# Optimization experiments

Hardware: AMD Instinct MI355X
Metric: run time of the kernel (lower is better)

## Reference

```python
import jax, jax.numpy as jnp
import numpy as np

N, B, H, L, FE = 32768, 256, 128, 4, 4
E = 262144


def setup_inputs() -> dict:
    key = jax.random.key(0)
    ks = jax.random.split(key, 16)
    def g(i, shape, scale=0.05):
        return jax.random.normal(ks[i], shape, dtype=jnp.float32) * scale
    return {
        "d": jax.random.uniform(ks[0], (E,), dtype=jnp.float32) * 5.0,
        "src": jax.random.randint(ks[1], (E,), 0, N),
        "dst": jax.random.randint(ks[2], (E,), 0, N),
        "seg": jnp.sort(jax.random.randint(ks[3], (N,), 0, B)),
        "node_emb": g(4, (H,), 1.0),
        "We": g(5, (2 * FE + 1, H)), "be": jnp.zeros((H,), jnp.float32),
        "msg_W1": g(6, (L, 3 * H, H)), "msg_b1": jnp.zeros((L, H), jnp.float32),
        "msg_W2": g(7, (L, H, H)), "msg_b2": jnp.zeros((L, H), jnp.float32),
        "soft_W": g(8, (L, H)), "soft_b": jnp.zeros((L,), jnp.float32),
        "upd_W1": g(9, (L, H, H)), "upd_b1": jnp.zeros((L, H), jnp.float32),
        "upd_W2": g(10, (L, H, H)), "upd_b2": jnp.zeros((L, H), jnp.float32),
        "out_W1": g(11, (H, H)), "out_b1": jnp.zeros((H,), jnp.float32),
        "out_W2": g(12, (H, H)), "out_b2": jnp.zeros((H,), jnp.float32),
    }


def reference(d, src, dst, seg, node_emb, We, be, msg_W1, msg_b1, msg_W2, msg_b2,
              soft_W, soft_b, upd_W1, upd_b1, upd_W2, upd_b2,
              out_W1, out_b1, out_W2, out_b2):
    silu = jax.nn.silu
    # fourier_encode_dist: [E] -> [E, 2*FE+1] = [sin(d/2^k), cos(d/2^k), d]
    scales = 2.0 ** jnp.arange(FE, dtype=d.dtype)
    x = d[:, None] / scales
    de = jnp.concatenate([jnp.sin(x), jnp.cos(x), d[:, None]], axis=-1)
    # edge_input MLP (1 layer, last_activation=SiLU) then extra F.silu in input_edge_func
    e = silu(silu(de @ We + be))                              # [E, H]
    # node_embedding broadcast to all nodes
    feat = jnp.broadcast_to(node_emb, (N, H))
    for l in range(L):
        mi = jnp.concatenate([feat[src], feat[dst], e], axis=-1)        # [E, 3H]
        m = silu(silu(mi @ msg_W1[l] + msg_b1[l]) @ msg_W2[l] + msg_b2[l])  # [E, H]
        e = e + m                                             # edge residual update
        w = jax.nn.sigmoid(m @ soft_W[l] + soft_b[l])[:, None]  # soft edge gate [E,1]
        msum = jax.ops.segment_sum(m * w, dst, num_segments=N)  # reduce to dst nodes
        upd_in = msum + feat
        feat = silu(upd_in @ upd_W1[l] + upd_b1[l]) @ upd_W2[l] + upd_b2[l] + feat
    # node-wise output network (2 layers, last activation None)
    feat = silu(feat @ out_W1 + out_b1) @ out_W2 + out_b2
    # multi-aggregator readout over graphs in batch
    s = jax.ops.segment_sum(feat, seg, num_segments=B)
    cnt = jax.ops.segment_sum(jnp.ones((N, 1), feat.dtype), seg, num_segments=B)
    mean = s / jnp.maximum(cnt, 1.0)
    mx = jax.ops.segment_max(feat, seg, num_segments=B)
    return jnp.concatenate([s, mean, mx], axis=-1)            # [B, 3H]
```

## Files before the change

kernel.cpp:

```cpp
#include <hip/hip_runtime.h>
#include <hip/hip_bf16.h>

#define NN 32768
#define NB 256
#define HD 128
#define NL 4
#define NE 262144

typedef short bf16x8 __attribute__((ext_vector_type(8)));
typedef float f32x4 __attribute__((ext_vector_type(4)));
typedef unsigned short u16;
typedef unsigned int u32;

__device__ __forceinline__ float bf2f(u16 u) {
  return __uint_as_float(((u32)u) << 16);
}
__device__ __forceinline__ u16 f2bf(float f) {
  u32 x = __float_as_uint(f);
  u32 r = x + 0x7FFFu + ((x >> 16) & 1u);
  return (u16)(r >> 16);
}
__device__ __forceinline__ u32 pk2(float a, float b) {
  __hip_bfloat162 h = __float22bfloat162_rn(make_float2(a, b));
  return *reinterpret_cast<u32*>(&h);
}
__device__ __forceinline__ float siluf(float x) {
  return x * __builtin_amdgcn_rcpf(1.0f + __expf(-x));
}
__device__ __forceinline__ float sigf(float x) {
  return __builtin_amdgcn_rcpf(1.0f + __expf(-x));
}
__device__ __forceinline__ u32 ordu(float f) {
  u32 b = __float_as_uint(f);
  return (b & 0x80000000u) ? ~b : (b | 0x80000000u);
}

__device__ __forceinline__ float ldinf(const void* p, size_t i, int mode) {
  return mode ? ((const float*)p)[i] : bf2f(((const u16*)p)[i]);
}
__device__ __forceinline__ u16 ldinb(const void* p, size_t i, int mode) {
  return mode ? f2bf(((const float*)p)[i]) : ((const u16*)p)[i];
}

__global__ void k_detect(const u16* __restrict__ Weraw, int* __restrict__ flag) {
  if (threadIdx.x == 0 && blockIdx.x == 0) {
    int cnt = 0;
    for (int i = 0; i < 256; i++) {
      u16 u = Weraw[2 * i];
      u32 e = (u >> 7) & 0xFFu;
      if (e >= 112u && e <= 126u) cnt++;
    }
    *flag = (cnt >= 128) ? 0 : 1;
  }
}

__global__ void k_v0(const void* __restrict__ nemb, const void* __restrict__ mW1,
                     const int* __restrict__ flagp, float* __restrict__ v0f) {
  const int mode = *flagp;
  const int n = threadIdx.x;
  float s = 0.f;
  for (int k = 0; k < 256; k++)
    s += ldinf(nemb, k & 127, mode) * ldinf(mW1, (size_t)k * HD + n, mode);
  v0f[n] = s;
}

#define PANEL 16384

__global__ __launch_bounds__(256) void k_csr_deg(const int* __restrict__ dstp,
                                                 u32* __restrict__ deg) {
  const int i = blockIdx.x * 256 + threadIdx.x;
  atomicAdd(&deg[dstp[i]], 1u);
}

__global__ __launch_bounds__(1024) void k_csr_scan(const u32* __restrict__ deg,
                                                   int* __restrict__ rowptr,
                                                   int* __restrict__ cursor) {
  __shared__ int part[1024];
  const int t = threadIdx.x;
  int loc[32];
  int s = 0;
#pragma unroll
  for (int j = 0; j < 32; j++) { loc[j] = s; s += (int)deg[t * 32 + j]; }
  part[t] = s;
  __syncthreads();
  int inc = s;
  for (int off = 1; off < 1024; off <<= 1) {
    int tmp = (t >= off) ? part[t - off] : 0;
    __syncthreads();
    part[t] += tmp;
    __syncthreads();
  }
  const int base = part[t] - inc;
#pragma unroll
  for (int j = 0; j < 32; j++) {
    rowptr[t * 32 + j] = base + loc[j];
    cursor[t * 32 + j] = base + loc[j];
  }
  if (t == 1023) rowptr[NN] = part[1023];
}

__global__ __launch_bounds__(256) void k_csr_scatter(const int* __restrict__ dstp,
                                                     const int* __restrict__ srcp,
                                                     int* __restrict__ cursor,
                                                     int* __restrict__ eids,
                                                     int* __restrict__ src_s,
                                                     int* __restrict__ dst_s) {
  const int i = blockIdx.x * 256 + threadIdx.x;
  const int d = dstp[i];
  const int pos = atomicAdd(&cursor[d], 1);
  eids[pos] = i;
  src_s[pos] = srcp[i];
  dst_s[pos] = d;
}

template <int MT>
__device__ __forceinline__ void acc_zero(f32x4 (&acc)[MT][8]) {
#pragma unroll
  for (int mt = 0; mt < MT; mt++)
#pragma unroll
    for (int nt = 0; nt < 8; nt++) acc[mt][nt] = f32x4{0.f, 0.f, 0.f, 0.f};
}

__device__ __forceinline__ void load_a2(const u16* __restrict__ A0,
                                        const size_t* rowoff, int kg,
                                        bf16x8 (&a)[2][4]) {
#pragma unroll
  for (int ks = 0; ks < 4; ks++)
#pragma unroll
    for (int mt = 0; mt < 2; mt++)
      a[mt][ks] = *(const bf16x8*)&A0[rowoff[mt] + ks * 32 + kg * 8];
}

__device__ __forceinline__ void gemm_lds2(const bf16x8 (&a)[2][4],
                                          const short* sB, int l,
                                          f32x4 (&acc)[2][8]) {
#pragma unroll
  for (int ks = 0; ks < 4; ks++)
#pragma unroll
    for (int nt = 0; nt < 8; nt++) {
      bf16x8 b = *(const bf16x8*)&sB[((nt * 4 + ks) * 64 + l) * 8];
#pragma unroll
      for (int mt = 0; mt < 2; mt++)
        acc[mt][nt] = __builtin_amdgcn_mfma_f32_16x16x32_bf16(a[mt][ks], b, acc[mt][nt], 0, 0, 0);
    }
}

template <int MT>
__device__ __forceinline__ void wave_gemm_p(const short* lAw, const u16* __restrict__ Bp,
                                            int l, int c, int kg, f32x4 (&acc)[MT][8]) {
#pragma unroll
  for (int ks = 0; ks < 4; ks++) {
    bf16x8 a[MT];
#pragma unroll
    for (int mt = 0; mt < MT; mt++) {
      const int r = mt * 16 + c;
      const int k = ks * 32 + kg * 8;
      a[mt] = *(const bf16x8*)&lAw[r * HD + (k ^ ((r & 7) << 3))];
    }
#pragma unroll
    for (int nt = 0; nt < 8; nt++) {
      bf16x8 b = *(const bf16x8*)&Bp[(size_t)((nt * 4 + ks) * 64 + l) * 8];
#pragma unroll
      for (int mt = 0; mt < MT; mt++)
        acc[mt][nt] = __builtin_amdgcn_mfma_f32_16x16x32_bf16(a[mt], b, acc[mt][nt], 0, 0, 0);
    }
  }
}

template <int MT, bool SILU>
__device__ __forceinline__ void wave_pack(short* lAw, int c, int kg,
                                          f32x4 (&acc)[MT][8], const float* bias) {
#pragma unroll
  for (int mt = 0; mt < MT; mt++) {
#pragma unroll
    for (int rr = 0; rr < 4; rr++) {
      const int row = mt * 16 + kg * 4 + rr;
      u32 ou[4];
#pragma unroll
      for (int p = 0; p < 4; p++) {
        float x0 = acc[mt][2 * p][rr] + bias[2 * p];
        float x1 = acc[mt][2 * p + 1][rr] + bias[2 * p + 1];
        if (SILU) { x0 = siluf(x0); x1 = siluf(x1); }
        ou[p] = pk2(x0, x1);
      }
      ((int4*)(lAw + row * HD))[c ^ (row & 7)] =
          make_int4((int)ou[0], (int)ou[1], (int)ou[2], (int)ou[3]);
    }
  }
}

__device__ __forceinline__ void stage_panel(const u16* __restrict__ P,
                                            short* sB, int tid) {
#pragma unroll
  for (int it = 0; it < 8; it++) {
    const int idx = (it * 256 + tid) * 8;
    *(int4*)&sB[idx] = *(const int4*)&P[idx];
  }
}

__global__ __launch_bounds__(256) void k_prep(
    const void* __restrict__ mW1, const void* __restrict__ mW2,
    const void* __restrict__ uW1, const void* __restrict__ uW2,
    const void* __restrict__ oW1, const void* __restrict__ oW2,
    const int* __restrict__ flagp,
    u16* __restrict__ Wt1, u16* __restrict__ Wt2p,
    u16* __restrict__ Wtu1, u16* __restrict__ Wtu2p,
    u16* __restrict__ Wto1, u16* __restrict__ Wto2p) {
  const int mode = *flagp;
  const int tid = blockIdx.x * blockDim.x + threadIdx.x;
  const int stride = gridDim.x * blockDim.x;
  for (int i = tid; i < NL * 3 * PANEL; i += stride) {
    const int l = i / (3 * PANEL), r = i % (3 * PANEL);
    const int chunk = r / PANEL, r2 = r % PANEL;
    const int nt = r2 / 2048, ks = (r2 % 2048) / 512;
    const int lane = (r2 % 512) / 8, j = r2 % 8;
    const int s = ks * 32 + (lane >> 4) * 8 + j;
    const int klog = ((s & 7) << 4) | (s >> 3);
    const int n = nt * 16 + (lane & 15);
    Wt1[i] = ldinb(mW1, ((size_t)l * 384 + chunk * 128 + klog) * HD + n, mode);
  }
  for (int i = tid; i < NL * PANEL; i += stride) {
    const int l = i / PANEL, r = i % PANEL;
    const int nt = r / 2048, ks = (r % 2048) / 512;
    const int lane = (r % 512) / 8, j = r % 8;
    const int s = ks * 32 + (lane >> 4) * 8 + j;
    const int klog = ((s & 7) << 4) | (s >> 3);
    const int n = nt * 16 + (lane & 15);
    Wt2p[i] = ldinb(mW2, ((size_t)l * HD + klog) * HD + n, mode);
    Wtu1[i] = ldinb(uW1, ((size_t)l * HD + klog) * HD + n, mode);
    Wtu2p[i] = ldinb(uW2, ((size_t)l * HD + klog) * HD + n, mode);
  }
  for (int i = tid; i < PANEL; i += stride) {
    const int nt = i / 2048, ks = (i % 2048) / 512;
    const int lane = (i % 512) / 8, j = i % 8;
    const int s = ks * 32 + (lane >> 4) * 8 + j;
    const int klog = ((s & 7) << 4) | (s >> 3);
    const int n = nt * 16 + (lane & 15);
    Wto1[i] = ldinb(oW1, (size_t)klog * HD + n, mode);
    Wto2p[i] = ldinb(oW2, (size_t)klog * HD + n, mode);
  }
}

__global__ __launch_bounds__(256) void k_featinit(const void* __restrict__ nemb,
                                                  const int* __restrict__ flagp,
                                                  u16* __restrict__ feat) {
  const int mode = *flagp;
  const int i = blockIdx.x * 256 + threadIdx.x;
  const int g = i & 15;
  u32 ou[4];
#pragma unroll
  for (int p = 0; p < 4; p++) {
    u16 a = ldinb(nemb, (2 * p) * 16 + g, mode);
    u16 b = ldinb(nemb, (2 * p + 1) * 16 + g, mode);
    ou[p] = (u32)a | ((u32)b << 16);
  }
  ((int4*)feat)[i] = make_int4((int)ou[0], (int)ou[1], (int)ou[2], (int)ou[3]);
}

__global__ __launch_bounds__(256) void k_encode(const void* __restrict__ d,
                                                const int* __restrict__ eids,
                                                const void* __restrict__ We,
                                                const void* __restrict__ be,
                                                const int* __restrict__ flagp,
                                                u16* __restrict__ e) {
  const int mode = *flagp;
  __shared__ float sW[9 * HD];
  __shared__ float sb[HD];
  for (int i = threadIdx.x; i < 9 * HD; i += 256) sW[i] = ldinf(We, i, mode);
  for (int i = threadIdx.x; i < HD; i += 256) sb[i] = ldinf(be, i, mode);
  __syncthreads();
  const int spos = blockIdx.x * 256 + threadIdx.x;
  const float dv = ldinf(d, eids[spos], mode);
  float de[9];
#pragma unroll
  for (int k = 0; k < 4; k++) {
    float x = dv * (1.0f / (float)(1 << k));
    de[k] = __sinf(x);
    de[4 + k] = __cosf(x);
  }
  de[8] = dv;
  u16* erow = e + (size_t)spos * HD;
#pragma unroll
  for (int g = 0; g < 16; g++) {
    u32 ou[4];
#pragma unroll
    for (int p = 0; p < 4; p++) {
      float vv[2];
#pragma unroll
      for (int t = 0; t < 2; t++) {
        const int h = (2 * p + t) * 16 + g;
        float a = sb[h];
#pragma unroll
        for (int k = 0; k < 9; k++) a += de[k] * sW[k * HD + h];
        vv[t] = siluf(siluf(a));
      }
      ou[p] = pk2(vv[0], vv[1]);
    }
    ((int4*)erow)[g] = make_int4((int)ou[0], (int)ou[1], (int)ou[2], (int)ou[3]);
  }
}

template <bool FIRST>
__global__ __launch_bounds__(256, 2) void k_edge(
    const u16* __restrict__ feat, u16* __restrict__ e,
    const int* __restrict__ src_s, const int* __restrict__ dst_s,
    const u16* __restrict__ Wt1, const u16* __restrict__ Wt2p,
    const void* __restrict__ b1g, const void* __restrict__ b2g,
    const void* __restrict__ softW, const void* __restrict__ softb,
    const int* __restrict__ flagp, const float* __restrict__ v0f,
    float* __restrict__ msum, int layer) {
  __shared__ __align__(16) short sB[PANEL];
  __shared__ __align__(16) short lM[128 * HD];
  __shared__ float swg[128];
  __shared__ int sdst[128];
  const int mode = *flagp;
  const int tid = threadIdx.x;
  const int l = tid & 63, wid = tid >> 6;
  const int c = l & 15, kg = l >> 4;
  const int bid = (int)blockIdx.x;
  const int blkB = (((bid & 7) << 8) | (bid >> 3)) * 128;
  const int blk = blkB + wid * 32;
  short* lMw = lM + wid * 32 * HD;
  float* swgw = swg + wid * 32;
  int* sdstw = sdst + wid * 32;

  if (l < 32) sdstw[l] = dst_s[blk + l];

  size_t offS[2], offD[2], offE[2];
#pragma unroll
  for (int mt = 0; mt < 2; mt++) {
    const int eidx = blk + mt * 16 + c;
    if (!FIRST) {
      offS[mt] = (size_t)src_s[eidx] * HD;
      offD[mt] = (size_t)dst_s[eidx] * HD;
    }
    offE[mt] = (size_t)eidx * HD;
  }

  const u16* W1l = Wt1 + (size_t)layer * 3 * PANEL;
  const u16* W2l = Wt2p + (size_t)layer * PANEL;
  float bias1[8], bias2[8], swf[8];
#pragma unroll
  for (int nt = 0; nt < 8; nt++) {
    bias1[nt] = ldinf(b1g, layer * HD + nt * 16 + c, mode);
    if (FIRST) bias1[nt] += v0f[nt * 16 + c];
    bias2[nt] = ldinf(b2g, layer * HD + nt * 16 + c, mode);
    swf[nt] = ldinf(softW, (size_t)layer * HD + nt * 16 + c, mode);
  }
  const float sbv = ldinf(softb, layer, mode);

  f32x4 acc[2][8];
  acc_zero<2>(acc);
  bf16x8 a[2][4];

  if (!FIRST) {
    load_a2(feat, offS, kg, a);
    stage_panel(W1l, sB, tid);
    __syncthreads();
    gemm_lds2(a, sB, l, acc);
    __syncthreads();
    load_a2(feat, offD, kg, a);
    stage_panel(W1l + PANEL, sB, tid);
    __syncthreads();
    gemm_lds2(a, sB, l, acc);
    __syncthreads();
  }
  load_a2(e, offE, kg, a);
  stage_panel(W1l + 2 * PANEL, sB, tid);
  __syncthreads();
  gemm_lds2(a, sB, l, acc);
  __syncthreads();

  stage_panel(W2l, sB, tid);
  wave_pack<2, true>(lMw, c, kg, acc, bias1);
  __syncthreads();

  acc_zero<2>(acc);
  wave_gemm_p<2>(lMw, (const u16*)sB, l, c, kg, acc);

  float wred[2][4];
#pragma unroll
  for (int mt = 0; mt < 2; mt++) {
#pragma unroll
    for (int rr = 0; rr < 4; rr++) {
      const int row = mt * 16 + kg * 4 + rr;
      int4* erow4 = (int4*)(e + (size_t)(blk + row) * HD);
      const int4 eo = erow4[c];
      const u32 eu[4] = {(u32)eo.x, (u32)eo.y, (u32)eo.z, (u32)eo.w};
      float mv[8];
      float wp = 0.f;
#pragma unroll
      for (int nt = 0; nt < 8; nt++) {
        mv[nt] = siluf(acc[mt][nt][rr] + bias2[nt]);
        wp += mv[nt] * swf[nt];
      }
      u32 mo[4], ou[4];
#pragma unroll
      for (int p = 0; p < 4; p++) {
        mo[p] = pk2(mv[2 * p], mv[2 * p + 1]);
        ou[p] = pk2(bf2f((u16)(eu[p] & 0xffffu)) + mv[2 * p],
                    bf2f((u16)(eu[p] >> 16)) + mv[2 * p + 1]);
      }
      ((int4*)(lMw + row * HD))[c ^ (row & 7)] =
          make_int4((int)mo[0], (int)mo[1], (int)mo[2], (int)mo[3]);
      erow4[c] = make_int4((int)ou[0], (int)ou[1], (int)ou[2], (int)ou[3]);
      wp += __shfl_xor(wp, 1);
      wp += __shfl_xor(wp, 2);
      wp += __shfl_xor(wp, 4);
      wp += __shfl_xor(wp, 8);
      wred[mt][rr] = wp;
    }
  }
#pragma unroll
  for (int mt = 0; mt < 2; mt++)
#pragma unroll
    for (int rr = 0; rr < 4; rr++)
      if (c == mt * 4 + rr) swgw[mt * 16 + kg * 4 + rr] = sigf(wred[mt][rr] + sbv);

  const int gM = ((l >> 3) << 3);
  const int em = l & 7;
  float a0 = 0.f, a1 = 0.f;
  int cur = sdstw[0];
  for (int r = 0; r < 32; r++) {
    const int dn = sdstw[r];
    if (dn != cur) {
      atomicAdd(&msum[(size_t)cur * HD + l], a0);
      atomicAdd(&msum[(size_t)cur * HD + l + 64], a1);
      a0 = 0.f; a1 = 0.f; cur = dn;
    }
    const int rx = (r & 7) << 3;
    const float wgr = swgw[r];
    a0 += wgr * bf2f((u16)lMw[r * HD + (gM ^ rx) + em]);
    a1 += wgr * bf2f((u16)lMw[r * HD + (gM ^ rx) + 64 + em]);
  }
  atomicAdd(&msum[(size_t)cur * HD + l], a0);
  atomicAdd(&msum[(size_t)cur * HD + l + 64], a1);
}

template <bool LAST>
__global__ __launch_bounds__(64, 4) void k_node(
    u16* __restrict__ feat, float* __restrict__ msum,
    const u16* __restrict__ Wtu1, const u16* __restrict__ Wtu2p,
    const void* __restrict__ b1g, const void* __restrict__ b2g,
    const int* __restrict__ flagp, int layer,
    const int* __restrict__ seg,
    const u16* __restrict__ Wto1, const u16* __restrict__ Wto2p,
    const void* __restrict__ ob1, const void* __restrict__ ob2,
    float* __restrict__ sacc, u32* __restrict__ mxacc, float* __restrict__ cnt) {
  __shared__ __align__(16) short lA[32 * HD];
  __shared__ int sseg[32];
  const int mode = *flagp;
  const int l = threadIdx.x;
  const int c = l & 15, kg = l >> 4;
  short* lAw = lA;
  const int bid = (int)blockIdx.x;
  const int blkn = (((bid & 7) << 7) | (bid >> 3)) * 32;
  const u16* W1l = Wtu1 + (size_t)layer * PANEL;
  const u16* W2l = Wtu2p + (size_t)layer * PANEL;
  float bias1[8], bias2[8];
#pragma unroll
  for (int nt = 0; nt < 8; nt++) {
    bias1[nt] = ldinf(b1g, layer * HD + nt * 16 + c, mode);
    bias2[nt] = ldinf(b2g, layer * HD + nt * 16 + c, mode);
  }
  if (LAST && l < 32) sseg[l] = seg[blkn + l];

  const float4 z4 = make_float4(0.f, 0.f, 0.f, 0.f);
#pragma unroll
  for (int rp = 0; rp < 8; rp++) {
    const int r = rp * 4 + (l >> 4);
    const int g = l & 15;
    const int4 fv = ((const int4*)(feat + (size_t)(blkn + r) * HD))[g];
    const u32 uu[4] = {(u32)fv.x, (u32)fv.y, (u32)fv.z, (u32)fv.w};
    float4* mrow4 = (float4*)(msum + (size_t)(blkn + r) * HD);
    const float4 ma = mrow4[2 * g];
    const float4 mb = mrow4[2 * g + 1];
    mrow4[2 * g] = z4;
    mrow4[2 * g + 1] = z4;
    const float mm[8] = {ma.x, ma.y, ma.z, ma.w, mb.x, mb.y, mb.z, mb.w};
    u32 ou[4];
#pragma unroll
    for (int p = 0; p < 4; p++) {
      ou[p] = pk2(bf2f((u16)(uu[p] & 0xffffu)) + mm[2 * p],
                  bf2f((u16)(uu[p] >> 16)) + mm[2 * p + 1]);
    }
    ((int4*)(lAw + r * HD))[g ^ (r & 7)] =
        make_int4((int)ou[0], (int)ou[1], (int)ou[2], (int)ou[3]);
  }
  __syncthreads();
  f32x4 acc[2][8];
  acc_zero<2>(acc);
  wave_gemm_p<2>(lAw, W1l, l, c, kg, acc);
  __syncthreads();
  wave_pack<2, true>(lAw, c, kg, acc, bias1);
  __syncthreads();
  acc_zero<2>(acc);
  wave_gemm_p<2>(lAw, W2l, l, c, kg, acc);
  __syncthreads();

#pragma unroll
  for (int mt = 0; mt < 2; mt++) {
#pragma unroll
    for (int rr = 0; rr < 4; rr++) {
      const int row = mt * 16 + kg * 4 + rr;
      int4* frow4 = (int4*)(feat + (size_t)(blkn + row) * HD);
      const int4 fo = frow4[c];
      const u32 fu[4] = {(u32)fo.x, (u32)fo.y, (u32)fo.z, (u32)fo.w};
      u32 ou[4];
#pragma unroll
      for (int p = 0; p < 4; p++) {
        const float x0 = acc[mt][2 * p][rr] + bias2[2 * p];
        const float x1 = acc[mt][2 * p + 1][rr] + bias2[2 * p + 1];
        ou[p] = pk2(bf2f((u16)(fu[p] & 0xffffu)) + x0,
                    bf2f((u16)(fu[p] >> 16)) + x1);
      }
      const int4 nv = make_int4((int)ou[0], (int)ou[1], (int)ou[2], (int)ou[3]);
      if (LAST) {
        ((int4*)(lAw + row * HD))[c ^ (row & 7)] = nv;
      } else {
        frow4[c] = nv;
      }
    }
  }

  if (LAST) {
    __syncthreads();
    float ob1r[8], ob2r[8];
#pragma unroll
    for (int nt = 0; nt < 8; nt++) {
      ob1r[nt] = ldinf(ob1, nt * 16 + c, mode);
      ob2r[nt] = ldinf(ob2, nt * 16 + c, mode);
    }
    acc_zero<2>(acc);
    wave_gemm_p<2>(lAw, Wto1, l, c, kg, acc);
    __syncthreads();
    wave_pack<2, true>(lAw, c, kg, acc, ob1r);
    __syncthreads();
    acc_zero<2>(acc);
    wave_gemm_p<2>(lAw, Wto2p, l, c, kg, acc);
    __syncthreads();
    wave_pack<2, false>(lAw, c, kg, acc, ob2r);
    __syncthreads();

    const int gL = l >> 2;
    const int eoff = (l & 3) * 2;
    const bool uniform = (sseg[0] == sseg[31]);
    if (uniform) {
      const int g = sseg[0];
      float s1 = 0.f, s2 = 0.f, x1 = -3.402823e38f, x2 = -3.402823e38f;
#pragma unroll 4
      for (int r = 0; r < 32; r++) {
        const u32 mv = *(const u32*)&lAw[r * HD + ((gL ^ (r & 7)) << 3) + eoff];
        const float v1 = bf2f((u16)(mv & 0xffffu));
        const float v2 = bf2f((u16)(mv >> 16));
        s1 += v1; s2 += v2;
        x1 = fmaxf(x1, v1); x2 = fmaxf(x2, v2);
      }
      atomicAdd(&sacc[(size_t)g * HD + 2 * l], s1);
      atomicAdd(&sacc[(size_t)g * HD + 2 * l + 1], s2);
      atomicMax(&mxacc[(size_t)g * HD + 2 * l], ordu(x1));
      atomicMax(&mxacc[(size_t)g * HD + 2 * l + 1], ordu(x2));
      if (l == 0) atomicAdd(&cnt[g], 32.0f);
    } else {
      if (l < 32) atomicAdd(&cnt[sseg[l]], 1.0f);
#pragma unroll 4
      for (int r = 0; r < 32; r++) {
        const u32 mv = *(const u32*)&lAw[r * HD + ((gL ^ (r & 7)) << 3) + eoff];
        const float v1 = bf2f((u16)(mv & 0xffffu));
        const float v2 = bf2f((u16)(mv >> 16));
        const int g = sseg[r];
        atomicAdd(&sacc[(size_t)g * HD + 2 * l], v1);
        atomicAdd(&sacc[(size_t)g * HD + 2 * l + 1], v2);
        atomicMax(&mxacc[(size_t)g * HD + 2 * l], ordu(v1));
        atomicMax(&mxacc[(size_t)g * HD + 2 * l + 1], ordu(v2));
      }
    }
  }
}

__global__ __launch_bounds__(256) void k_final(const float* __restrict__ sacc,
                                               const u32* __restrict__ mxacc,
                                               const float* __restrict__ cnt,
                                               const int* __restrict__ flagp,
                                               void* __restrict__ out) {
  const int mode = *flagp;
  const int i = blockIdx.x * 256 + threadIdx.x;
  const int b = i / 384, j = i % 384;
  float v;
  if (j < HD) {
    const int p = ((j & 15) << 3) | (j >> 4);
    v = sacc[b * HD + p];
  } else if (j < 2 * HD) {
    const int t = j - HD;
    const int p = ((t & 15) << 3) | (t >> 4);
    v = sacc[b * HD + p] / fmaxf(cnt[b], 1.0f);
  } else {
    const int t = j - 2 * HD;
    const int p = ((t & 15) << 3) | (t >> 4);
    u32 u = mxacc[b * HD + p];
    u32 bits = (u >> 31) ? (u ^ 0x80000000u) : ~u;
    v = __uint_as_float(bits);
  }
  if (mode) ((float*)out)[i] = v;
  else ((u16*)out)[i] = f2bf(v);
}

extern "C" void kernel_launch(void* const* d_in, const int* in_sizes, int n_in,
                              void* d_out, int out_size, void* d_ws, size_t ws_size,
                              hipStream_t stream) {
  const void* d_d = d_in[0];
  const int* src = (const int*)d_in[1];
  const int* dst = (const int*)d_in[2];
  const int* seg = (const int*)d_in[3];
  const void* nemb = d_in[4];
  const void* We = d_in[5];
  const void* be = d_in[6];
  const void* mW1 = d_in[7];
  const void* mb1 = d_in[8];
  const void* mW2 = d_in[9];
  const void* mb2 = d_in[10];
  const void* sW = d_in[11];
  const void* sb = d_in[12];
  const void* uW1 = d_in[13];
  const void* ub1 = d_in[14];
  const void* uW2 = d_in[15];
  const void* ub2 = d_in[16];
  const void* oW1 = d_in[17];
  const void* ob1 = d_in[18];
  const void* oW2 = d_in[19];
  const void* ob2 = d_in[20];

  char* ws = (char*)d_ws;
  const size_t OFF_E = 0;
  const size_t OFF_MSUM = OFF_E + (size_t)NE * HD * 2;
  const size_t OFF_FEAT = OFF_MSUM + (size_t)NN * HD * 4;
  const size_t OFF_SACC = OFF_FEAT + (size_t)NN * HD * 2;
  const size_t OFF_MX = OFF_SACC + (size_t)NB * HD * 4;
  const size_t OFF_CNT = OFF_MX + (size_t)NB * HD * 4;
  const size_t OFF_DEG = OFF_CNT + 1024;
  const size_t OFF_ROWPTR = OFF_DEG + (size_t)NN * 4;
  const size_t OFF_CURSOR = OFF_ROWPTR + (size_t)(NN + 2) * 4;
  const size_t OFF_EIDS = OFF_CURSOR + (size_t)NN * 4;
  const size_t OFF_SRCS = OFF_EIDS + (size_t)NE * 4;
  const size_t OFF_DSTS = OFF_SRCS + (size_t)NE * 4;
  const size_t OFF_WT1 = OFF_DSTS + (size_t)NE * 4;
  const size_t OFF_WT2P = OFF_WT1 + (size_t)NL * 3 * PANEL * 2;
  const size_t OFF_WTU1 = OFF_WT2P + (size_t)NL * PANEL * 2;
  const size_t OFF_WTU2P = OFF_WTU1 + (size_t)NL * PANEL * 2;
  const size_t OFF_WTO1 = OFF_WTU2P + (size_t)NL * PANEL * 2;
  const size_t OFF_WTO2P = OFF_WTO1 + (size_t)PANEL * 2;
  const size_t OFF_FLAG = OFF_WTO2P + (size_t)PANEL * 2;
  const size_t OFF_V0 = OFF_FLAG + 64;

  u16* e = (u16*)(ws + OFF_E);
  float* msum = (float*)(ws + OFF_MSUM);
  u16* feat = (u16*)(ws + OFF_FEAT);
  float* sacc = (float*)(ws + OFF_SACC);
  u32* mx = (u32*)(ws + OFF_MX);
  float* cnt = (float*)(ws + OFF_CNT);
  u32* deg = (u32*)(ws + OFF_DEG);
  int* rowptr = (int*)(ws + OFF_ROWPTR);
  int* cursor = (int*)(ws + OFF_CURSOR);
  int* eids = (int*)(ws + OFF_EIDS);
  int* src_s = (int*)(ws + OFF_SRCS);
  int* dst_s = (int*)(ws + OFF_DSTS);
  u16* Wt1 = (u16*)(ws + OFF_WT1);
  u16* Wt2p = (u16*)(ws + OFF_WT2P);
  u16* Wtu1 = (u16*)(ws + OFF_WTU1);
  u16* Wtu2p = (u16*)(ws + OFF_WTU2P);
  u16* Wto1 = (u16*)(ws + OFF_WTO1);
  u16* Wto2p = (u16*)(ws + OFF_WTO2P);
  int* flag = (int*)(ws + OFF_FLAG);
  float* v0f = (float*)(ws + OFF_V0);

  hipMemsetAsync(ws + OFF_SACC, 0,
                 (size_t)NB * HD * 4 * 2 + 1024 + (size_t)NN * 4, stream);
  hipMemsetAsync(msum, 0, (size_t)NN * HD * 4, stream);

  k_detect<<<1, 64, 0, stream>>>((const u16*)We, flag);
  k_v0<<<1, 128, 0, stream>>>(nemb, mW1, flag, v0f);
  k_prep<<<256, 256, 0, stream>>>(mW1, mW2, uW1, uW2, oW1, oW2, flag,
                                  Wt1, Wt2p, Wtu1, Wtu2p, Wto1, Wto2p);
  k_featinit<<<(NN * HD / 8) / 256, 256, 0, stream>>>(nemb, flag, feat);

  k_csr_deg<<<NE / 256, 256, 0, stream>>>(dst, deg);
  k_csr_scan<<<1, 1024, 0, stream>>>(deg, rowptr, cursor);
  k_csr_scatter<<<NE / 256, 256, 0, stream>>>(dst, src, cursor, eids, src_s, dst_s);

  k_encode<<<NE / 256, 256, 0, stream>>>(d_d, eids, We, be, flag, e);

  for (int l = 0; l < NL; l++) {
    if (l == 0)
      k_edge<true><<<NE / 128, 256, 0, stream>>>(feat, e, src_s, dst_s, Wt1, Wt2p,
                                                 mb1, mb2, sW, sb, flag, v0f, msum, l);
    else
      k_edge<false><<<NE / 128, 256, 0, stream>>>(feat, e, src_s, dst_s, Wt1, Wt2p,
                                                  mb1, mb2, sW, sb, flag, v0f, msum, l);
    if (l < NL - 1)
      k_node<false><<<NN / 32, 64, 0, stream>>>(feat, msum, Wtu1, Wtu2p, ub1, ub2,
                                                flag, l, seg, Wto1, Wto2p, ob1, ob2,
                                                sacc, mx, cnt);
    else
      k_node<true><<<NN / 32, 64, 0, stream>>>(feat, msum, Wtu1, Wtu2p, ub1, ub2,
                                               flag, l, seg, Wto1, Wto2p, ob1, ob2,
                                               sacc, mx, cnt);
  }
  k_final<<<(NB * 384) / 256, 256, 0, stream>>>(sacc, mx, cnt, flag, d_out);
}
```

Before: 717.9 us.

## Fuse CSR scatter with edge encode, merge detect kernels, shrink edge LDS

Merges the format-detect and v0 kernels into one launch, and fuses the CSR scatter with the Fourier edge encoding so each edge's features are written straight to its sorted position, dropping the eids array and its indirect load. In k_edge the second-layer weight panel is no longer staged into LDS. The per-wave packed intermediate reuses the weight panel buffer, and the second GEMM reads W2 directly from global memory. The occupancy hint rises from 2 to 4 blocks per CU. This trades LDS reuse of W2 for higher occupancy, but the scattered e-row writes and global W2 reads may cost bandwidth.

```diff
diff --git a/kernel.cpp b/kernel.cpp
--- a/kernel.cpp
+++ b/kernel.cpp
@@ -42,21 +42,24 @@
   return mode ? f2bf(((const float*)p)[i]) : ((const u16*)p)[i];
 }
 
-__global__ void k_detect(const u16* __restrict__ Weraw, int* __restrict__ flag) {
-  if (threadIdx.x == 0 && blockIdx.x == 0) {
+__global__ void k_detect_v0(const u16* __restrict__ Weraw,
+                            const void* __restrict__ nemb,
+                            const void* __restrict__ mW1,
+                            int* __restrict__ flag, float* __restrict__ v0f) {
+  __shared__ int smode;
+  if (threadIdx.x == 0) {
     int cnt = 0;
     for (int i = 0; i < 256; i++) {
       u16 u = Weraw[2 * i];
       u32 e = (u >> 7) & 0xFFu;
       if (e >= 112u && e <= 126u) cnt++;
     }
-    *flag = (cnt >= 128) ? 0 : 1;
-  }
-}
-
-__global__ void k_v0(const void* __restrict__ nemb, const void* __restrict__ mW1,
-                     const int* __restrict__ flagp, float* __restrict__ v0f) {
-  const int mode = *flagp;
+    const int m = (cnt >= 128) ? 0 : 1;
+    *flag = m;
+    smode = m;
+  }
+  __syncthreads();
+  const int mode = smode;
   const int n = threadIdx.x;
   float s = 0.f;
   for (int k = 0; k < 256; k++)
@@ -99,18 +102,51 @@
   if (t == 1023) rowptr[NN] = part[1023];
 }
 
-__global__ __launch_bounds__(256) void k_csr_scatter(const int* __restrict__ dstp,
-                                                     const int* __restrict__ srcp,
-                                                     int* __restrict__ cursor,
-                                                     int* __restrict__ eids,
-                                                     int* __restrict__ src_s,
-                                                     int* __restrict__ dst_s) {
+__global__ __launch_bounds__(256) void k_scatter_encode(
+    const int* __restrict__ dstp, const int* __restrict__ srcp,
+    int* __restrict__ cursor, int* __restrict__ src_s, int* __restrict__ dst_s,
+    const void* __restrict__ d, const void* __restrict__ We,
+    const void* __restrict__ be, const int* __restrict__ flagp,
+    u16* __restrict__ e) {
+  const int mode = *flagp;
+  __shared__ float sW[9 * HD];
+  __shared__ float sb[HD];
+  for (int i = threadIdx.x; i < 9 * HD; i += 256) sW[i] = ldinf(We, i, mode);
+  for (int i = threadIdx.x; i < HD; i += 256) sb[i] = ldinf(be, i, mode);
+  __syncthreads();
   const int i = blockIdx.x * 256 + threadIdx.x;
-  const int d = dstp[i];
-  const int pos = atomicAdd(&cursor[d], 1);
-  eids[pos] = i;
+  const int dn = dstp[i];
+  const int pos = atomicAdd(&cursor[dn], 1);
   src_s[pos] = srcp[i];
-  dst_s[pos] = d;
+  dst_s[pos] = dn;
+  const float dv = ldinf(d, i, mode);
+  float de[9];
+#pragma unroll
+  for (int k = 0; k < 4; k++) {
+    float x = dv * (1.0f / (float)(1 << k));
+    de[k] = __sinf(x);
+    de[4 + k] = __cosf(x);
+  }
+  de[8] = dv;
+  u16* erow = e + (size_t)pos * HD;
+#pragma unroll
+  for (int g = 0; g < 16; g++) {
+    u32 ou[4];
+#pragma unroll
+    for (int p = 0; p < 4; p++) {
+      float vv[2];
+#pragma unroll
+      for (int t = 0; t < 2; t++) {
+        const int h = (2 * p + t) * 16 + g;
+        float a = sb[h];
+#pragma unroll
+        for (int k = 0; k < 9; k++) a += de[k] * sW[k * HD + h];
+        vv[t] = siluf(siluf(a));
+      }
+      ou[p] = pk2(vv[0], vv[1]);
+    }
+    ((int4*)erow)[g] = make_int4((int)ou[0], (int)ou[1], (int)ou[2], (int)ou[3]);
+  }
 }
 
 template <int MT>
@@ -257,51 +293,8 @@
   ((int4*)feat)[i] = make_int4((int)ou[0], (int)ou[1], (int)ou[2], (int)ou[3]);
 }
 
-__global__ __launch_bounds__(256) void k_encode(const void* __restrict__ d,
-                                                const int* __restrict__ eids,
-                                                const void* __restrict__ We,
-                                                const void* __restrict__ be,
-                                                const int* __restrict__ flagp,
-                                                u16* __restrict__ e) {
-  const int mode = *flagp;
-  __shared__ float sW[9 * HD];
-  __shared__ float sb[HD];
-  for (int i = threadIdx.x; i < 9 * HD; i += 256) sW[i] = ldinf(We, i, mode);
-  for (int i = threadIdx.x; i < HD; i += 256) sb[i] = ldinf(be, i, mode);
-  __syncthreads();
-  const int spos = blockIdx.x * 256 + threadIdx.x;
-  const float dv = ldinf(d, eids[spos], mode);
-  float de[9];
-#pragma unroll
-  for (int k = 0; k < 4; k++) {
-    float x = dv * (1.0f / (float)(1 << k));
-    de[k] = __sinf(x);
-    de[4 + k] = __cosf(x);
-  }
-  de[8] = dv;
-  u16* erow = e + (size_t)spos * HD;
-#pragma unroll
-  for (int g = 0; g < 16; g++) {
-    u32 ou[4];
-#pragma unroll
-    for (int p = 0; p < 4; p++) {
-      float vv[2];
-#pragma unroll
-      for (int t = 0; t < 2; t++) {
-        const int h = (2 * p + t) * 16 + g;
-        float a = sb[h];
-#pragma unroll
-        for (int k = 0; k < 9; k++) a += de[k] * sW[k * HD + h];
-        vv[t] = siluf(siluf(a));
-      }
-      ou[p] = pk2(vv[0], vv[1]);
-    }
-    ((int4*)erow)[g] = make_int4((int)ou[0], (int)ou[1], (int)ou[2], (int)ou[3]);
-  }
-}
-
 template <bool FIRST>
-__global__ __launch_bounds__(256, 2) void k_edge(
+__global__ __launch_bounds__(256, 4) void k_edge(
     const u16* __restrict__ feat, u16* __restrict__ e,
     const int* __restrict__ src_s, const int* __restrict__ dst_s,
     const u16* __restrict__ Wt1, const u16* __restrict__ Wt2p,
@@ -310,7 +303,6 @@
     const int* __restrict__ flagp, const float* __restrict__ v0f,
     float* __restrict__ msum, int layer) {
   __shared__ __align__(16) short sB[PANEL];
-  __shared__ __align__(16) short lM[128 * HD];
   __shared__ float swg[128];
   __shared__ int sdst[128];
   const int mode = *flagp;
@@ -320,7 +312,7 @@
   const int bid = (int)blockIdx.x;
   const int blkB = (((bid & 7) << 8) | (bid >> 3)) * 128;
   const int blk = blkB + wid * 32;
-  short* lMw = lM + wid * 32 * HD;
+  short* lMw = sB + wid * 32 * HD;
   float* swgw = swg + wid * 32;
   int* sdstw = sdst + wid * 32;
 
@@ -371,12 +363,10 @@
   gemm_lds2(a, sB, l, acc);
   __syncthreads();
 
-  stage_panel(W2l, sB, tid);
   wave_pack<2, true>(lMw, c, kg, acc, bias1);
-  __syncthreads();
 
   acc_zero<2>(acc);
-  wave_gemm_p<2>(lMw, (const u16*)sB, l, c, kg, acc);
+  wave_gemm_p<2>(lMw, W2l, l, c, kg, acc);
 
   float wred[2][4];
 #pragma unroll
@@ -640,8 +630,7 @@
   const size_t OFF_DEG = OFF_CNT + 1024;
   const size_t OFF_ROWPTR = OFF_DEG + (size_t)NN * 4;
   const size_t OFF_CURSOR = OFF_ROWPTR + (size_t)(NN + 2) * 4;
-  const size_t OFF_EIDS = OFF_CURSOR + (size_t)NN * 4;
-  const size_t OFF_SRCS = OFF_EIDS + (size_t)NE * 4;
+  const size_t OFF_SRCS = OFF_CURSOR + (size_t)NN * 4;
   const size_t OFF_DSTS = OFF_SRCS + (size_t)NE * 4;
   const size_t OFF_WT1 = OFF_DSTS + (size_t)NE * 4;
   const size_t OFF_WT2P = OFF_WT1 + (size_t)NL * 3 * PANEL * 2;
@@ -661,7 +650,6 @@
   u32* deg = (u32*)(ws + OFF_DEG);
   int* rowptr = (int*)(ws + OFF_ROWPTR);
   int* cursor = (int*)(ws + OFF_CURSOR);
-  int* eids = (int*)(ws + OFF_EIDS);
   int* src_s = (int*)(ws + OFF_SRCS);
   int* dst_s = (int*)(ws + OFF_DSTS);
   u16* Wt1 = (u16*)(ws + OFF_WT1);
@@ -677,17 +665,15 @@
                  (size_t)NB * HD * 4 * 2 + 1024 + (size_t)NN * 4, stream);
   hipMemsetAsync(msum, 0, (size_t)NN * HD * 4, stream);
 
-  k_detect<<<1, 64, 0, stream>>>((const u16*)We, flag);
-  k_v0<<<1, 128, 0, stream>>>(nemb, mW1, flag, v0f);
+  k_detect_v0<<<1, 128, 0, stream>>>((const u16*)We, nemb, mW1, flag, v0f);
   k_prep<<<256, 256, 0, stream>>>(mW1, mW2, uW1, uW2, oW1, oW2, flag,
                                   Wt1, Wt2p, Wtu1, Wtu2p, Wto1, Wto2p);
   k_featinit<<<(NN * HD / 8) / 256, 256, 0, stream>>>(nemb, flag, feat);
 
   k_csr_deg<<<NE / 256, 256, 0, stream>>>(dst, deg);
   k_csr_scan<<<1, 1024, 0, stream>>>(deg, rowptr, cursor);
-  k_csr_scatter<<<NE / 256, 256, 0, stream>>>(dst, src, cursor, eids, src_s, dst_s);
-
-  k_encode<<<NE / 256, 256, 0, stream>>>(d_d, eids, We, be, flag, e);
+  k_scatter_encode<<<NE / 256, 256, 0, stream>>>(dst, src, cursor, src_s, dst_s,
+                                                 d_d, We, be, flag, e);
 
   for (int l = 0; l < NL; l++) {
     if (l == 0)
```

New measurement: 680.3 us. -5.2%, faster.
